# Kernel tuning notes

Measured on AMD Instinct MI355X. Metric: run time of the kernel, lower is better.

The kernel has to match this reference:

```python
import jax, jax.numpy as jnp
import numpy as np

# Irreps layout: x = [32x0e | 16x1o] -> dim 32 + 48 = 80; sh = [1x0e | 1x1o] -> dim 4
MUL0, MUL1 = 32, 16
DIM = MUL0 + 3 * MUL1            # 80
E, N = 100000, 10000             # edges, nodes
EDGE_DIM, HIDDEN = 32, 64
# e3nn instruction order (i_in1 outer, i_in2 inner):
#   A: 0e x 0e -> 0e  (MUL0*MUL0)
#   C: 0e x 1o -> 1o  (MUL0*MUL1)
#   D: 1o x 0e -> 1o  (MUL1*MUL1)
#   B: 1o x 1o -> 0e  (MUL1*MUL0)
NA = MUL0 * MUL0
NC = MUL0 * MUL1
ND = MUL1 * MUL1
NB = MUL1 * MUL0
WNUM = NA + NC + ND + NB         # tp.weight_numel = 2304
INV_SQRT3 = 1.0 / np.sqrt(3.0).astype(np.float32)   # CG (1,1,0) = delta/sqrt(3)
NORM = np.float32(1.0 / np.sqrt(MUL0 + MUL1))        # element path norm: fan-in = 32+16 = 48 for both outputs


def setup_inputs() -> dict:
    key = jax.random.key(0)
    ks = jax.random.split(key, 10)
    return {
        "dst": jax.random.randint(ks[0], (E,), 0, N),
        "x_src": jax.random.normal(ks[1], (E, DIM), jnp.float32),
        "x_dst": jax.random.normal(ks[2], (N, DIM), jnp.float32),
        "sh": jax.random.normal(ks[3], (E, 4), jnp.float32),
        "edge_attr": jax.random.normal(ks[4], (E, EDGE_DIM), jnp.float32),
        "mlp_w1": jax.random.normal(ks[5], (EDGE_DIM, HIDDEN), jnp.float32) / np.sqrt(EDGE_DIM),
        "mlp_b1": jnp.zeros((HIDDEN,), jnp.float32),
        "mlp_w2": jax.random.normal(ks[6], (HIDDEN, WNUM), jnp.float32) / np.sqrt(HIDDEN),
        "mlp_b2": jnp.zeros((WNUM,), jnp.float32),
        "res_w0": jax.random.normal(ks[7], (MUL0, MUL0), jnp.float32),
        "res_w1": jax.random.normal(ks[8], (MUL1, MUL1), jnp.float32),
    }


def reference(dst, x_src, x_dst, sh, edge_attr, mlp_w1, mlp_b1, mlp_w2, mlp_b2, res_w0, res_w1):
    e = x_src.shape[0]
    n = x_dst.shape[0]
    # edge MLP -> per-edge tensor-product weights
    h = jax.nn.relu(edge_attr @ mlp_w1 + mlp_b1)
    w = h @ mlp_w2 + mlp_b2                              # [E, WNUM]
    wa = w[:, :NA].reshape(e, MUL0, MUL0)                # 0e x 0e -> 0e
    wc = w[:, NA:NA + NC].reshape(e, MUL0, MUL1)         # 0e x 1o -> 1o
    wd = w[:, NA + NC:NA + NC + ND].reshape(e, MUL1, MUL1)  # 1o x 0e -> 1o
    wb = w[:, NA + NC + ND:].reshape(e, MUL1, MUL0)      # 1o x 1o -> 0e

    x0 = x_src[:, :MUL0]                                 # [E, 32]
    x1 = x_src[:, MUL0:].reshape(e, MUL1, 3)             # [E, 16, 3]
    sh0 = sh[:, 0]                                       # [E]
    sh1 = sh[:, 1:4]                                     # [E, 3]

    # equivariant tensor product with per-edge weights
    out0 = NORM * (jnp.einsum('euw,eu,e->ew', wa, x0, sh0)
                   + INV_SQRT3 * jnp.einsum('euw,eum,em->ew', wb, x1, sh1))   # [E, 32]
    out1 = NORM * (jnp.einsum('euw,eu,em->ewm', wc, x0, sh1)
                   + jnp.einsum('euw,eum,e->ewm', wd, x1, sh0))               # [E, 16, 3]
    msg = jnp.concatenate([out0, out1.reshape(e, 3 * MUL1)], axis=-1)        # [E, 80]

    # scatter-mean to destination nodes
    sums = jax.ops.segment_sum(msg, dst, num_segments=n)                      # [N, 80]
    cnt = jax.ops.segment_sum(jnp.ones((e,), msg.dtype), dst, num_segments=n)
    mean = sums / jnp.maximum(cnt, 1.0)[:, None]

    # residual: e3nn Linear (per-irrep, fan-in normalized)
    r0 = (x_dst[:, :MUL0] @ res_w0) / np.sqrt(MUL0)
    r1 = jnp.einsum('num,uw->nwm', x_dst[:, MUL0:].reshape(n, MUL1, 3), res_w1) / np.sqrt(MUL1)
    res = jnp.concatenate([r0, r1.reshape(n, 3 * MUL1)], axis=-1)

    return res + mean
```

## Files before the change

### kernel.cpp

```cpp
#include <hip/hip_runtime.h>
#include <hip/hip_bf16.h>

#define E_TOT   100000
#define N_NODES 10000
#define DIMV    80
#define HID     64
#define EDIM    32
#define WNUM    2304
#define TE      32

static constexpr float NORMF      = 0.14433756729740643f;
static constexpr float INV_SQRT3F = 0.57735026918962576f;
static constexpr float RS32       = 0.17677669529663687f;
static constexpr float RS16       = 0.25f;

typedef __attribute__((ext_vector_type(8))) short bf16x8;
typedef __attribute__((ext_vector_type(4))) float f32x4;

static __device__ __forceinline__ ushort f2bf(float v) {
    __hip_bfloat16 h(v);
    return *reinterpret_cast<ushort*>(&h);
}

__global__ __launch_bounds__(256) void prep_w2t(const float* __restrict__ W2,
                                                ushort* __restrict__ W2T) {
    __shared__ float sT[64][65];
    const int j0 = blockIdx.x * 64;
    #pragma unroll
    for (int k = 0; k < 16; ++k) {
        int idx = threadIdx.x + k*256;
        int t = idx >> 6, j = idx & 63;
        sT[j][t] = W2[t*WNUM + j0 + j];
    }
    __syncthreads();
    #pragma unroll
    for (int k = 0; k < 16; ++k) {
        int idx = threadIdx.x + k*256;
        int j = idx >> 6, t = idx & 63;
        W2T[(size_t)(j0 + j)*64 + t] = f2bf(sT[j][t]);
    }
}

__global__ __launch_bounds__(256, 4) void edge_kernel(
    const int* __restrict__ dst, const float* __restrict__ x_src,
    const float* __restrict__ sh, const float* __restrict__ ea,
    const float* __restrict__ W1, const float* __restrict__ b1,
    const ushort* __restrict__ W2T, const float* __restrict__ b2,
    float* __restrict__ sums, float* __restrict__ cnt)
{
    __shared__ float  sX[TE][81];
    __shared__ float  sSh[TE][4];
    __shared__ float  sXs1[TE][17];
    __shared__ float  sEcA[TE][33];
    __shared__ ushort sHbf[TE][HID];
    __shared__ float  sMsg[TE][84];
    __shared__ int    sDst[TE];

    const int tid  = threadIdx.x;
    const int lane = tid & 63;
    const int wave = tid >> 6;
    const int e0   = blockIdx.x * TE;

    for (int i = tid; i < TE*DIMV; i += 256) { int e = i/80, k = i-e*80; sX[e][k] = x_src[e0*DIMV + i]; }
    for (int i = tid; i < TE*EDIM; i += 256) { int e = i>>5, k = i&31; sEcA[e][k] = ea[e0*EDIM + i]; }
    for (int i = tid; i < TE*4;    i += 256) sSh[0][i] = sh[e0*4 + i];
    if (tid < TE) sDst[tid] = dst[e0 + tid];
    __syncthreads();

    #pragma unroll
    for (int k = 0; k < (TE*HID)/256; ++k) {
        int idx = tid + k*256;
        int e = idx >> 6, t = idx & 63;
        float h = b1[t];
        #pragma unroll
        for (int i = 0; i < EDIM; ++i) h = fmaf(sEcA[e][i], W1[i*HID + t], h);
        sHbf[e][t] = f2bf(fmaxf(h, 0.f));
    }
    __syncthreads();

    for (int i = tid; i < TE*32; i += 256) {
        int e = i >> 5, u = i & 31;
        sEcA[e][u] = sSh[e][0] * sX[e][u];
    }
    for (int i = tid; i < TE*16; i += 256) {
        int e = i >> 4, u = i & 15;
        sXs1[e][u] = INV_SQRT3F * (sX[e][32+u*3+0]*sSh[e][1] +
                                   sX[e][32+u*3+1]*sSh[e][2] +
                                   sX[e][32+u*3+2]*sSh[e][3]);
    }
    for (int i = tid; i < TE*84; i += 256) sMsg[0][i] = 0.f;
    __syncthreads();

    const int c     = lane & 15;
    const int g     = lane >> 4;
    const int rbase = g << 2;
    bf16x8 afrag[2][2];
    #pragma unroll
    for (int rt = 0; rt < 2; ++rt)
        #pragma unroll
        for (int kt = 0; kt < 2; ++kt)
            afrag[rt][kt] = *reinterpret_cast<const bf16x8*>(&sHbf[rt*16 + c][kt*32 + g*8]);

    float pA[8]     = {};
    float sC2[8]    = {};
    float sDv[8][3] = {};

    auto tile_mfma = [&](int t16, f32x4& a0, f32x4& a1) {
        const int j0 = t16 << 4;
        const ushort* bp = W2T + (((size_t)(j0 + c)) << 6) + (g << 3);
        bf16x8 bf0 = *reinterpret_cast<const bf16x8*>(bp);
        bf16x8 bf1 = *reinterpret_cast<const bf16x8*>(bp + 32);
        const float bv = b2[j0 + c];
        a0 = {bv, bv, bv, bv};
        a1 = {bv, bv, bv, bv};
        a0 = __builtin_amdgcn_mfma_f32_16x16x32_bf16(afrag[0][0], bf0, a0, 0, 0, 0);
        a0 = __builtin_amdgcn_mfma_f32_16x16x32_bf16(afrag[0][1], bf1, a0, 0, 0, 0);
        a1 = __builtin_amdgcn_mfma_f32_16x16x32_bf16(afrag[1][0], bf0, a1, 0, 0, 0);
        a1 = __builtin_amdgcn_mfma_f32_16x16x32_bf16(afrag[1][1], bf1, a1, 0, 0, 0);
    };

    #pragma unroll 2
    for (int k = 0; k < 16; ++k) {
        const int t16 = wave + (k << 2);
        f32x4 a0, a1; tile_mfma(t16, a0, a1);
        const int u = t16 >> 1;
        #pragma unroll
        for (int r = 0; r < 4; ++r) {
            pA[r]   = fmaf(sEcA[rbase + r][u],      a0[r], pA[r]);
            pA[4+r] = fmaf(sEcA[16 + rbase + r][u], a1[r], pA[4+r]);
        }
    }
    #pragma unroll 2
    for (int k = 0; k < 8; ++k) {
        const int t16 = 64 + wave + (k << 2);
        f32x4 a0, a1; tile_mfma(t16, a0, a1);
        const int u = t16 - 64;
        #pragma unroll
        for (int r = 0; r < 4; ++r) {
            sC2[r]   = fmaf(sX[rbase + r][u],      a0[r], sC2[r]);
            sC2[4+r] = fmaf(sX[16 + rbase + r][u], a1[r], sC2[4+r]);
        }
    }
    #pragma unroll
    for (int k = 0; k < 4; ++k) {
        const int t16 = 96 + wave + (k << 2);
        f32x4 a0, a1; tile_mfma(t16, a0, a1);
        const int u = t16 - 96;
        #pragma unroll
        for (int r = 0; r < 4; ++r) {
            #pragma unroll
            for (int m = 0; m < 3; ++m) {
                sDv[r][m]   = fmaf(sX[rbase + r][32 + u*3 + m],      a0[r], sDv[r][m]);
                sDv[4+r][m] = fmaf(sX[16 + rbase + r][32 + u*3 + m], a1[r], sDv[4+r][m]);
            }
        }
    }
    #pragma unroll 2
    for (int k = 0; k < 8; ++k) {
        const int t16 = 112 + wave + (k << 2);
        f32x4 a0, a1; tile_mfma(t16, a0, a1);
        const int u = (t16 - 112) >> 1;
        #pragma unroll
        for (int r = 0; r < 4; ++r) {
            pA[r]   = fmaf(sXs1[rbase + r][u],      a0[r], pA[r]);
            pA[4+r] = fmaf(sXs1[16 + rbase + r][u], a1[r], pA[4+r]);
        }
    }

    const int wcol = c + ((wave & 1) << 4);
    #pragma unroll
    for (int rt = 0; rt < 2; ++rt) {
        #pragma unroll
        for (int r = 0; r < 4; ++r) {
            const int e = rt*16 + rbase + r;
            const int s = rt*4 + r;
            atomicAdd(&sMsg[e][wcol], pA[s]);
            const float s0 = sSh[e][0];
            atomicAdd(&sMsg[e][32 + c*3 + 0], sSh[e][1]*sC2[s] + s0*sDv[s][0]);
            atomicAdd(&sMsg[e][32 + c*3 + 1], sSh[e][2]*sC2[s] + s0*sDv[s][1]);
            atomicAdd(&sMsg[e][32 + c*3 + 2], sSh[e][3]*sC2[s] + s0*sDv[s][2]);
        }
    }
    __syncthreads();

    for (int i = tid; i < TE*DIMV; i += 256) {
        int e = i / DIMV, k = i - e*DIMV;
        atomicAdd(&sums[sDst[e]*DIMV + k], NORMF * sMsg[e][k]);
    }
    if (tid < TE) atomicAdd(&cnt[sDst[tid]], 1.0f);
}

__global__ __launch_bounds__(256) void node_kernel(
    const float* __restrict__ x_dst, const float* __restrict__ rw0,
    const float* __restrict__ rw1, const float* __restrict__ sums,
    const float* __restrict__ cnt, float* __restrict__ out)
{
    int gid = blockIdx.x*256 + threadIdx.x;
    if (gid >= N_NODES*DIMV) return;
    int n = gid / DIMV;
    int k = gid - n*DIMV;
    const float* xd = x_dst + n*DIMV;
    float r = 0.f;
    if (k < 32) {
        #pragma unroll
        for (int u = 0; u < 32; ++u) r = fmaf(xd[u], rw0[u*32 + k], r);
        r *= RS32;
    } else {
        int kk = k - 32;
        int w = kk / 3, m = kk - w*3;
        #pragma unroll
        for (int u = 0; u < 16; ++u) r = fmaf(xd[32 + u*3 + m], rw1[u*16 + w], r);
        r *= RS16;
    }
    float cc = cnt[n];
    out[gid] = r + sums[gid] / fmaxf(cc, 1.f);
}

extern "C" void kernel_launch(void* const* d_in, const int* in_sizes, int n_in,
                              void* d_out, int out_size, void* d_ws, size_t ws_size,
                              hipStream_t stream) {
    const int*   dst   = (const int*)  d_in[0];
    const float* x_src = (const float*)d_in[1];
    const float* x_dst = (const float*)d_in[2];
    const float* sh    = (const float*)d_in[3];
    const float* ea    = (const float*)d_in[4];
    const float* W1    = (const float*)d_in[5];
    const float* b1    = (const float*)d_in[6];
    const float* W2    = (const float*)d_in[7];
    const float* b2    = (const float*)d_in[8];
    const float* rw0   = (const float*)d_in[9];
    const float* rw1   = (const float*)d_in[10];
    float* out  = (float*)d_out;

    float*  sums = (float*)d_ws;
    float*  cnt  = sums + (size_t)N_NODES*DIMV;
    ushort* W2T  = (ushort*)((char*)d_ws + (size_t)(N_NODES*DIMV + N_NODES)*sizeof(float));

    hipMemsetAsync(d_ws, 0, (size_t)(N_NODES*DIMV + N_NODES)*sizeof(float), stream);
    prep_w2t<<<WNUM/64, 256, 0, stream>>>(W2, W2T);
    edge_kernel<<<E_TOT/TE, 256, 0, stream>>>(dst, x_src, sh, ea, W1, b1, W2T, b2, sums, cnt);
    node_kernel<<<(N_NODES*DIMV + 255)/256, 256, 0, stream>>>(x_dst, rw0, rw1, sums, cnt, out);
}
```

Before: 423.5 us.

## Replace atomic scatter-mean with CSR-sorted edge gather per node

Builds a CSR index of edges grouped by destination node (histogram, single-block scan, atomic-cursor scatter). The edge kernel then writes per-edge messages to a dense buffer instead of doing global float atomics, and the node kernel gathers and sums each node's messages. The aim is to remove contention from global atomics. In exchange it adds several small launches, a 32 MB message buffer written and read back, uncoalesced indirect gathers, and a serial single-block scan. It falls back to the old atomic path if the workspace is too small.

```diff
diff --git a/kernel.cpp b/kernel.cpp
--- a/kernel.cpp
+++ b/kernel.cpp
@@ -41,12 +41,58 @@
     }
 }
 
+__global__ __launch_bounds__(256) void hist_kernel(const int* __restrict__ dst,
+                                                   int* __restrict__ hist) {
+    int e = blockIdx.x*256 + threadIdx.x;
+    if (e < E_TOT) atomicAdd(&hist[dst[e]], 1);
+}
+
+__global__ __launch_bounds__(256) void scan_kernel(const int* __restrict__ hist,
+                                                   int* __restrict__ offs,
+                                                   float* __restrict__ cntf) {
+    __shared__ int part[256];
+    const int t = threadIdx.x;
+    const int base = t * 40;
+    int s = 0;
+    for (int i = 0; i < 40; ++i) { int n = base + i; if (n < N_NODES) s += hist[n]; }
+    part[t] = s; __syncthreads();
+    for (int d = 1; d < 256; d <<= 1) {
+        int v = 0; if (t >= d) v = part[t - d];
+        __syncthreads();
+        if (t >= d) part[t] += v;
+        __syncthreads();
+    }
+    int run = (t > 0) ? part[t-1] : 0;
+    for (int i = 0; i < 40; ++i) {
+        int n = base + i;
+        if (n < N_NODES) {
+            offs[n] = run;
+            int h = hist[n];
+            run += h;
+            cntf[n] = (float)(h > 0 ? h : 1);
+        }
+    }
+}
+
+__global__ __launch_bounds__(256) void scatter_kernel(const int* __restrict__ dst,
+                                                      int* __restrict__ cursor,
+                                                      const int* __restrict__ offs,
+                                                      int* __restrict__ eidx) {
+    int e = blockIdx.x*256 + threadIdx.x;
+    if (e < E_TOT) {
+        int d = dst[e];
+        int p = atomicAdd(&cursor[d], 1);
+        eidx[offs[d] + p] = e;
+    }
+}
+
+template<int MODE>
 __global__ __launch_bounds__(256, 4) void edge_kernel(
     const int* __restrict__ dst, const float* __restrict__ x_src,
     const float* __restrict__ sh, const float* __restrict__ ea,
     const float* __restrict__ W1, const float* __restrict__ b1,
     const ushort* __restrict__ W2T, const float* __restrict__ b2,
-    float* __restrict__ sums, float* __restrict__ cnt)
+    float* __restrict__ outbuf, float* __restrict__ cnt)
 {
     __shared__ float  sX[TE][81];
     __shared__ float  sSh[TE][4];
@@ -183,11 +229,48 @@
     }
     __syncthreads();
 
-    for (int i = tid; i < TE*DIMV; i += 256) {
-        int e = i / DIMV, k = i - e*DIMV;
-        atomicAdd(&sums[sDst[e]*DIMV + k], NORMF * sMsg[e][k]);
-    }
-    if (tid < TE) atomicAdd(&cnt[sDst[tid]], 1.0f);
+    if (MODE == 0) {
+        for (int i = tid; i < TE*DIMV; i += 256) {
+            int e = i / DIMV, k = i - e*DIMV;
+            atomicAdd(&outbuf[sDst[e]*DIMV + k], NORMF * sMsg[e][k]);
+        }
+        if (tid < TE) atomicAdd(&cnt[sDst[tid]], 1.0f);
+    } else {
+        for (int i = tid; i < TE*DIMV; i += 256) {
+            int e = i / DIMV, k = i - e*DIMV;
+            outbuf[(size_t)(e0 + e)*DIMV + k] = NORMF * sMsg[e][k];
+        }
+    }
+}
+
+__global__ __launch_bounds__(256) void node_gather_kernel(
+    const float* __restrict__ x_dst, const float* __restrict__ rw0,
+    const float* __restrict__ rw1, const float* __restrict__ msg,
+    const int* __restrict__ offs, const int* __restrict__ eidx,
+    const float* __restrict__ cntf, const int* __restrict__ hist,
+    float* __restrict__ out)
+{
+    int gid = blockIdx.x*256 + threadIdx.x;
+    if (gid >= N_NODES*DIMV) return;
+    int n = gid / DIMV;
+    int k = gid - n*DIMV;
+    const float* xd = x_dst + n*DIMV;
+    float r = 0.f;
+    if (k < 32) {
+        #pragma unroll
+        for (int u = 0; u < 32; ++u) r = fmaf(xd[u], rw0[u*32 + k], r);
+        r *= RS32;
+    } else {
+        int kk = k - 32;
+        int w = kk / 3, m = kk - w*3;
+        #pragma unroll
+        for (int u = 0; u < 16; ++u) r = fmaf(xd[32 + u*3 + m], rw1[u*16 + w], r);
+        r *= RS16;
+    }
+    float s = 0.f;
+    const int o = offs[n], d = hist[n];
+    for (int j = 0; j < d; ++j) s += msg[(size_t)eidx[o + j]*DIMV + k];
+    out[gid] = r + s / cntf[n];
 }
 
 __global__ __launch_bounds__(256) void node_kernel(
@@ -230,14 +313,45 @@
     const float* b2    = (const float*)d_in[8];
     const float* rw0   = (const float*)d_in[9];
     const float* rw1   = (const float*)d_in[10];
-    float* out  = (float*)d_out;
-
-    float*  sums = (float*)d_ws;
-    float*  cnt  = sums + (size_t)N_NODES*DIMV;
-    ushort* W2T  = (ushort*)((char*)d_ws + (size_t)(N_NODES*DIMV + N_NODES)*sizeof(float));
-
-    hipMemsetAsync(d_ws, 0, (size_t)(N_NODES*DIMV + N_NODES)*sizeof(float), stream);
-    prep_w2t<<<WNUM/64, 256, 0, stream>>>(W2, W2T);
-    edge_kernel<<<E_TOT/TE, 256, 0, stream>>>(dst, x_src, sh, ea, W1, b1, W2T, b2, sums, cnt);
-    node_kernel<<<(N_NODES*DIMV + 255)/256, 256, 0, stream>>>(x_dst, rw0, rw1, sums, cnt, out);
-}
+    float* out = (float*)d_out;
+    char*  ws  = (char*)d_ws;
+
+    size_t off = 0;
+    auto alloc = [&](size_t bytes) { size_t o = off; off = (off + bytes + 255) & ~255ULL; return o; };
+    size_t o_w2t  = alloc((size_t)WNUM*HID*2);
+    size_t o_hist = alloc((size_t)N_NODES*4);
+    size_t o_offs = alloc((size_t)N_NODES*4);
+    size_t o_cur  = alloc((size_t)N_NODES*4);
+    size_t o_eidx = alloc((size_t)E_TOT*4);
+    size_t o_cntf = alloc((size_t)N_NODES*4);
+    size_t o_msg  = alloc((size_t)E_TOT*DIMV*4);
+    const bool use_csr = (off <= ws_size);
+
+    if (use_csr) {
+        ushort* W2T   = (ushort*)(ws + o_w2t);
+        int*    histp = (int*)   (ws + o_hist);
+        int*    offsp = (int*)   (ws + o_offs);
+        int*    curp  = (int*)   (ws + o_cur);
+        int*    eidx  = (int*)   (ws + o_eidx);
+        float*  cntf  = (float*) (ws + o_cntf);
+        float*  msg   = (float*) (ws + o_msg);
+
+        hipMemsetAsync(histp, 0, (size_t)N_NODES*4, stream);
+        hipMemsetAsync(curp,  0, (size_t)N_NODES*4, stream);
+        prep_w2t<<<WNUM/64, 256, 0, stream>>>(W2, W2T);
+        hist_kernel<<<(E_TOT + 255)/256, 256, 0, stream>>>(dst, histp);
+        scan_kernel<<<1, 256, 0, stream>>>(histp, offsp, cntf);
+        scatter_kernel<<<(E_TOT + 255)/256, 256, 0, stream>>>(dst, curp, offsp, eidx);
+        edge_kernel<1><<<E_TOT/TE, 256, 0, stream>>>(dst, x_src, sh, ea, W1, b1, W2T, b2, msg, nullptr);
+        node_gather_kernel<<<(N_NODES*DIMV + 255)/256, 256, 0, stream>>>(
+            x_dst, rw0, rw1, msg, offsp, eidx, cntf, histp, out);
+    } else {
+        float*  sums = (float*)ws;
+        float*  cnt  = sums + (size_t)N_NODES*DIMV;
+        ushort* W2T  = (ushort*)(ws + (size_t)(N_NODES*DIMV + N_NODES)*sizeof(float));
+        hipMemsetAsync(ws, 0, (size_t)(N_NODES*DIMV + N_NODES)*sizeof(float), stream);
+        prep_w2t<<<WNUM/64, 256, 0, stream>>>(W2, W2T);
+        edge_kernel<0><<<E_TOT/TE, 256, 0, stream>>>(dst, x_src, sh, ea, W1, b1, W2T, b2, sums, cnt);
+        node_kernel<<<(N_NODES*DIMV + 255)/256, 256, 0, stream>>>(x_dst, rw0, rw1, sums, cnt, out);
+    }
+}
```

Result: slower. 480.2 us (+13.4%).
